# Kernel optimization log

Hardware: AMD Instinct MI355X
Metric: run time of the kernel (lower is better)

## Reference

```python
import jax, jax.numpy as jnp
import numpy as np

H = 768
NH = 12
HD = H // NH  # 64


def setup_inputs() -> dict:
    key = jax.random.key(0)
    ks = jax.random.split(key, 8)
    B, S = 4, 2048
    sc = 1.0 / np.sqrt(H)
    return {
        "hidden_states": jax.random.normal(ks[0], (B, S, H), dtype=jnp.float32),
        "attention_mask": jnp.zeros((B, 1, 1, S), dtype=jnp.float32),
        "Wq": jax.random.normal(ks[1], (H, H), dtype=jnp.float32) * sc,
        "bq": jnp.zeros((H,), dtype=jnp.float32),
        "Wk": jax.random.normal(ks[2], (H, H), dtype=jnp.float32) * sc,
        "bk": jnp.zeros((H,), dtype=jnp.float32),
        "Wv": jax.random.normal(ks[3], (H, H), dtype=jnp.float32) * sc,
        "bv": jnp.zeros((H,), dtype=jnp.float32),
    }


def _split_heads(x):
    # [B,S,H] -> [B,NH,S,HD]
    B, S, _ = x.shape
    return x.reshape(B, S, NH, HD).transpose(0, 2, 1, 3)


def reference(hidden_states, attention_mask, Wq, bq, Wk, bk, Wv, bv):
    q = _split_heads(hidden_states @ Wq + bq)
    k = _split_heads(hidden_states @ Wk + bk)
    v = _split_heads(hidden_states @ Wv + bv)
    # scores: [B,NH,S,S]
    scores = jnp.einsum("bhqd,bhkd->bhqk", q, k) / np.sqrt(HD)
    scores = scores + attention_mask
    probs = jax.nn.softmax(scores, axis=-1)  # dropout is identity in eval
    ctx = jnp.einsum("bhqk,bhkd->bhqd", probs, v)
    B, _, S, _ = ctx.shape
    return ctx.transpose(0, 2, 1, 3).reshape(B, S, H)
```

## Files before the change

kernel.cpp:

```cpp
#include <hip/hip_runtime.h>
#include <stdint.h>

typedef short bf16x8 __attribute__((ext_vector_type(8)));
typedef float f32x4  __attribute__((ext_vector_type(4)));
typedef float f32x16 __attribute__((ext_vector_type(16)));
typedef unsigned short u16;

#define B_  4
#define S_  2048
#define H_  768
#define NH_ 12
#define HD_ 64
#define NPROJ_N (3*H_)

static __device__ __forceinline__ u16 f2bf(float f) {
    union { float f; unsigned int u; } x; x.f = f;
    return (u16)((x.u + 0x8000u) >> 16);
}
static __device__ __forceinline__ bf16x8 ld8(const u16* p) {
    return *(const bf16x8*)(const void*)p;
}
static __device__ __forceinline__ void st8(u16* p, bf16x8 v) {
    *(bf16x8*)(void*)p = v;
}
static __device__ __forceinline__ void async_ld16(const u16* g, const short* l) {
    __builtin_amdgcn_global_load_lds(
        (__attribute__((address_space(1))) void*)g,
        (__attribute__((address_space(3))) void*)l,
        16, 0, 0);
}
static __device__ __forceinline__ unsigned cvtpk(float a, float b) {
    unsigned r;
    asm("v_cvt_pk_bf16_f32 %0, %1, %2" : "=v"(r) : "v"(a), "v"(b));
    return r;
}
static __device__ __forceinline__ void pl32swap(unsigned& a, unsigned& b) {
    asm("v_permlane32_swap_b32 %0, %1" : "+v"(a), "+v"(b));
}
static __device__ __forceinline__ bf16x8 mk8(unsigned a, unsigned b, unsigned c, unsigned d) {
    union { unsigned u[4]; bf16x8 v; } x;
    x.u[0] = a; x.u[1] = b; x.u[2] = c; x.u[3] = d;
    return x.v;
}

__global__ __launch_bounds__(256) void prep_kernel(const float* __restrict__ in,
                                                   u16* __restrict__ out,
                                                   const float* __restrict__ wq,
                                                   const float* __restrict__ wk,
                                                   const float* __restrict__ wv,
                                                   u16* __restrict__ wt,
                                                   const float* __restrict__ amask,
                                                   float* __restrict__ msc) {
    __shared__ float t[32][33];
    const int blk = blockIdx.x;
    const int tid = threadIdx.x;
    if (blk < 6144) {
        int i = (blk * 256 + tid) * 4;
        float4 v = *(const float4*)(in + i);
        ushort4 o;
        o.x = f2bf(v.x); o.y = f2bf(v.y); o.z = f2bf(v.z); o.w = f2bf(v.w);
        *(ushort4*)(out + i) = o;
    } else if (blk < 7872) {
        const int idx  = blk - 6144;
        const int proj = idx / 576;
        const int rem  = idx % 576;
        const int bx = rem % 24, by = rem / 24;
        const float* w = (proj == 0) ? wq : (proj == 1) ? wk : wv;
        u16* o = wt + (size_t)proj * H_ * H_;
        const int tx = tid & 31, ty = tid >> 5;
        const int n0 = bx * 32, k0 = by * 32;
        #pragma unroll
        for (int i = 0; i < 4; i++)
            t[ty + i * 8][tx] = w[(size_t)(k0 + ty + i * 8) * H_ + n0 + tx];
        __syncthreads();
        #pragma unroll
        for (int i = 0; i < 4; i++)
            o[(size_t)(n0 + ty + i * 8) * H_ + k0 + tx] = f2bf(t[tx][ty + i * 8]);
    } else {
        const int i = ((blk - 7872) * 256 + tid) * 8;
        float4 a0 = *(const float4*)(amask + i);
        float4 a1 = *(const float4*)(amask + i + 4);
        a0.x *= 1.44269504f; a0.y *= 1.44269504f; a0.z *= 1.44269504f; a0.w *= 1.44269504f;
        a1.x *= 1.44269504f; a1.y *= 1.44269504f; a1.z *= 1.44269504f; a1.w *= 1.44269504f;
        *(float4*)(msc + i)     = a0;
        *(float4*)(msc + i + 4) = a1;
    }
}

__global__ __launch_bounds__(256, 3) void qkv_gemm(const u16* __restrict__ A,
                                                   const u16* __restrict__ Wt,
                                                   const float* __restrict__ bq,
                                                   const float* __restrict__ bk,
                                                   const float* __restrict__ bv,
                                                   u16* __restrict__ qo,
                                                   u16* __restrict__ ko,
                                                   u16* __restrict__ vto) {
    __shared__ alignas(16) short SMEM[4][128 * 32];

    const int tid  = threadIdx.x;
    const int wave = tid >> 6;
    const int lane = tid & 63;
    const int quad = lane >> 4;
    const int l16  = lane & 15;
    const int wm   = wave & 1;
    const int wn   = wave >> 1;

    const int id  = blockIdx.x;
    const int xcd = id & 7;
    const int j   = id >> 3;
    const int mi  = j & 7;
    const int ni  = j >> 3;
    const int m0 = (xcd * 8 + mi) * 128;
    const int n0 = ni * 128;

    int stR[2], stC[2];
    #pragma unroll
    for (int jj = 0; jj < 2; jj++) {
        const int lc = jj * 256 + tid;
        stR[jj] = lc >> 2;
        stC[jj] = ((lc & 3) ^ ((lc >> 2) & 3)) * 8;
    }
    const int fx = (quad ^ (l16 & 3)) * 8;

    f32x4 acc[4][4];
    #pragma unroll
    for (int i = 0; i < 4; i++)
        #pragma unroll
        for (int jj = 0; jj < 4; jj++) acc[i][jj] = (f32x4)0.0f;

#define GSTAGE(kt_, buf_)                                                                     \
    do {                                                                                      \
        const int kk_ = (kt_) * 32;                                                           \
        _Pragma("unroll")                                                                     \
        for (int jj = 0; jj < 2; jj++) {                                                      \
            async_ld16(A  + (size_t)(m0 + stR[jj]) * H_ + kk_ + stC[jj],                      \
                       &SMEM[(buf_) * 2][(jj * 256 + tid) * 8]);                              \
            async_ld16(Wt + (size_t)(n0 + stR[jj]) * H_ + kk_ + stC[jj],                      \
                       &SMEM[(buf_) * 2 + 1][(jj * 256 + tid) * 8]);                          \
        }                                                                                     \
    } while (0)

    GSTAGE(0, 0);
    __syncthreads();

    for (int kt = 0; kt < 24; kt++) {
        const int cur = kt & 1;
        if (kt + 1 < 24) GSTAGE(kt + 1, cur ^ 1);
        const short* As = SMEM[cur * 2];
        const short* Bs = SMEM[cur * 2 + 1];
        bf16x8 af[4], bfr[4];
        #pragma unroll
        for (int i = 0; i < 4; i++)
            af[i] = *(const bf16x8*)(const void*)&As[(wm * 64 + i * 16 + l16) * 32 + fx];
        #pragma unroll
        for (int jj = 0; jj < 4; jj++)
            bfr[jj] = *(const bf16x8*)(const void*)&Bs[(wn * 64 + jj * 16 + l16) * 32 + fx];
        #pragma unroll
        for (int i = 0; i < 4; i++)
            #pragma unroll
            for (int jj = 0; jj < 4; jj++)
                acc[i][jj] = __builtin_amdgcn_mfma_f32_16x16x32_bf16(af[i], bfr[jj], acc[i][jj], 0, 0, 0);
        __syncthreads();
    }
#undef GSTAGE

    const int proj  = n0 / H_;
    const int hbase = (n0 % H_) >> 6;
    const float* bias = (proj == 0) ? bq : (proj == 1) ? bk : bv;
    u16* Ct = (u16*)SMEM;

    #pragma unroll
    for (int nj = 0; nj < 4; nj++) {
        const int nl = wn * 64 + nj * 16 + l16;
        const float bv_ = bias[(n0 % H_) + nl];
        #pragma unroll
        for (int mi2 = 0; mi2 < 4; mi2++) {
            #pragma unroll
            for (int r = 0; r < 4; r++) {
                const int ml = wm * 64 + mi2 * 16 + quad * 4 + r;
                const u16 val = f2bf(acc[mi2][nj][r] + bv_);
                if (proj < 2)
                    Ct[ml * 128 + ((nl + (ml & 15) * 8) & 127)] = val;
                else
                    Ct[nl * 128 + ((ml + (nl & 15) * 8) & 127)] = val;
            }
        }
    }
    __syncthreads();

    if (proj < 2) {
        u16* dst0 = (proj == 0) ? qo : ko;
        const int c = tid & 7;
        #pragma unroll
        for (int jj = 0; jj < 8; jj++) {
            const int idx = jj * 32 + (tid >> 3);
            const int ml = idx >> 1, h2 = idx & 1;
            const int nbase = h2 * 64 + c * 8;
            bf16x8 v8 = *(const bf16x8*)(const void*)&Ct[ml * 128 + ((nbase + (ml & 15) * 8) & 127)];
            const int m = m0 + ml;
            const int b = m >> 11, s = m & 2047;
            st8(dst0 + ((size_t)(b * NH_ + hbase + h2) * S_ + s) * HD_ + c * 8, v8);
        }
    } else {
        const int b = m0 >> 11;
        #pragma unroll
        for (int jj = 0; jj < 8; jj++) {
            const int nl = (tid >> 3) + (jj & 3) * 32;
            const int c  = (tid & 7) + (jj >> 2) * 8;
            bf16x8 v8 = *(const bf16x8*)(const void*)&Ct[nl * 128 + ((c * 8 + (nl & 15) * 8) & 127)];
            const int h2 = nl >> 6, d = nl & 63;
            st8(vto + ((size_t)(b * NH_ + hbase + h2) * HD_ + d) * S_ + (m0 & 2047) + c * 8, v8);
        }
    }
}

__global__ __launch_bounds__(256, 3) void attn_kernel(const u16* __restrict__ q,
                                                      const u16* __restrict__ k,
                                                      const u16* __restrict__ vt,
                                                      const float* __restrict__ msc,
                                                      float* __restrict__ out) {
    __shared__ alignas(16) short Ks[2][4096];
    __shared__ alignas(16) short Vs[2][4096];
    __shared__ alignas(16) float Ms[S_];

    const int tid  = threadIdx.x;
    const int wave = tid >> 6;
    const int lane = tid & 63;
    const int l32  = lane & 31;
    const int h    = lane >> 5;
    const int kh   = wave & 1;
    const int qg   = wave >> 1;

    const int bh = blockIdx.x;
    const int b  = bh / NH_;
    const int q0 = blockIdx.y * 128;
    const float C1 = 0.125f * 1.44269504f;

    {
        const float* mrow = msc + (size_t)b * S_;
        float4 a0 = *(const float4*)(mrow + tid * 8);
        float4 a1 = *(const float4*)(mrow + tid * 8 + 4);
        *(float4*)(Ms + tid * 8)     = a0;
        *(float4*)(Ms + tid * 8 + 4) = a1;
    }

    bf16x8 qf[2][4];
    #pragma unroll
    for (int qb = 0; qb < 2; qb++) {
        const u16* qrow = q + ((size_t)bh * S_ + q0 + qg * 64 + qb * 32 + l32) * HD_;
        #pragma unroll
        for (int i = 0; i < 4; i++) qf[qb][i] = ld8(qrow + i * 16 + h * 8);
    }

    const u16* kbase = k  + (size_t)bh * S_ * HD_;
    const u16* vbase = vt + (size_t)bh * HD_ * S_;

    const int sRow = tid >> 3;
    const int sCol = ((tid & 7) ^ (sRow & 7)) * 8;
    const int rx   = l32 & 7;

    float ls0 = 0.f, ls1 = 0.f;
    f32x16 oacc[2][2];
    #pragma unroll
    for (int qb = 0; qb < 2; qb++)
        #pragma unroll
        for (int dh = 0; dh < 2; dh++) oacc[qb][dh] = (f32x16)0.0f;

#define STAGE(kt_, buf_)                                                                           \
    do {                                                                                           \
        async_ld16(kbase + (size_t)(kt_) * 4096 + sRow * 64 + sCol,          &Ks[buf_][tid * 8]);  \
        async_ld16(kbase + (size_t)(kt_) * 4096 + (sRow + 32) * 64 + sCol,   &Ks[buf_][2048 + tid * 8]); \
        async_ld16(vbase + (size_t)sRow * S_ + (kt_) * 64 + sCol,            &Vs[buf_][tid * 8]);  \
        async_ld16(vbase + (size_t)(sRow + 32) * S_ + (kt_) * 64 + sCol,     &Vs[buf_][2048 + tid * 8]); \
    } while (0)

    STAGE(0, 0);
    __syncthreads();

    for (int kt = 0; kt < S_ / 64; kt++) {
        const int cur = kt & 1;
        if (kt + 1 < S_ / 64) STAGE(kt + 1, cur ^ 1);
        const short* Kc = Ks[cur];
        const short* Vc = Vs[cur];

        f32x16 s0 = (f32x16)0.0f;
        f32x16 s1 = (f32x16)0.0f;
        __builtin_amdgcn_s_setprio(1);
        #pragma unroll
        for (int i = 0; i < 4; i++) {
            bf16x8 kf = *(const bf16x8*)(const void*)&Kc[kh * 2048 + l32 * 64 + (((h + 2 * i) ^ rx) * 8)];
            s0 = __builtin_amdgcn_mfma_f32_32x32x16_bf16(kf, qf[0][i], s0, 0, 0, 0);
            s1 = __builtin_amdgcn_mfma_f32_32x32x16_bf16(kf, qf[1][i], s1, 0, 0, 0);
        }
        __builtin_amdgcn_s_setprio(0);

        unsigned w0[8], w1[8];
        #pragma unroll
        for (int c = 0; c < 4; c++) {
            const f32x4 mm = *(const f32x4*)&Ms[kt * 64 + kh * 32 + c * 8 + h * 4];
            const float p00 = __builtin_amdgcn_exp2f(__builtin_fmaf(s0[4*c+0], C1, mm[0]));
            const float p01 = __builtin_amdgcn_exp2f(__builtin_fmaf(s0[4*c+1], C1, mm[1]));
            const float p02 = __builtin_amdgcn_exp2f(__builtin_fmaf(s0[4*c+2], C1, mm[2]));
            const float p03 = __builtin_amdgcn_exp2f(__builtin_fmaf(s0[4*c+3], C1, mm[3]));
            const float p10 = __builtin_amdgcn_exp2f(__builtin_fmaf(s1[4*c+0], C1, mm[0]));
            const float p11 = __builtin_amdgcn_exp2f(__builtin_fmaf(s1[4*c+1], C1, mm[1]));
            const float p12 = __builtin_amdgcn_exp2f(__builtin_fmaf(s1[4*c+2], C1, mm[2]));
            const float p13 = __builtin_amdgcn_exp2f(__builtin_fmaf(s1[4*c+3], C1, mm[3]));
            w0[2*c]   = cvtpk(p00, p01);
            w0[2*c+1] = cvtpk(p02, p03);
            w1[2*c]   = cvtpk(p10, p11);
            w1[2*c+1] = cvtpk(p12, p13);
            ls0 += (p00 + p01) + (p02 + p03);
            ls1 += (p10 + p11) + (p12 + p13);
        }

        bf16x8 pa0[2], pa1[2];
        #pragma unroll
        for (int t = 0; t < 2; t++) {
            {
                unsigned a = w0[4*t+0], bb = w0[4*t+2];
                pl32swap(a, bb);
                unsigned c2 = w0[4*t+1], dd = w0[4*t+3];
                pl32swap(c2, dd);
                pa0[t] = mk8(a, c2, bb, dd);
            }
            {
                unsigned a = w1[4*t+0], bb = w1[4*t+2];
                pl32swap(a, bb);
                unsigned c2 = w1[4*t+1], dd = w1[4*t+3];
                pl32swap(c2, dd);
                pa1[t] = mk8(a, c2, bb, dd);
            }
        }

        __builtin_amdgcn_s_setprio(1);
        #pragma unroll
        for (int t = 0; t < 2; t++) {
            #pragma unroll
            for (int dh = 0; dh < 2; dh++) {
                bf16x8 vf = *(const bf16x8*)(const void*)&Vc[dh * 2048 + l32 * 64 + (((kh * 4 + 2 * t + h) ^ rx) * 8)];
                oacc[0][dh] = __builtin_amdgcn_mfma_f32_32x32x16_bf16(pa0[t], vf, oacc[0][dh], 0, 0, 0);
                oacc[1][dh] = __builtin_amdgcn_mfma_f32_32x32x16_bf16(pa1[t], vf, oacc[1][dh], 0, 0, 0);
            }
        }
        __builtin_amdgcn_s_setprio(0);
        __syncthreads();
    }
#undef STAGE

    ls0 += __shfl_xor(ls0, 32);
    ls1 += __shfl_xor(ls1, 32);

    float* R = qg ? (float*)Vs : (float*)Ks;

    if (kh == 1) {
        #pragma unroll
        for (int qb = 0; qb < 2; qb++)
            #pragma unroll
            for (int dh = 0; dh < 2; dh++)
                #pragma unroll
                for (int r = 0; r < 16; r++) {
                    const int qrow = (r & 3) + 8 * (r >> 2) + 4 * h;
                    R[(qb * 32 + qrow) * 64 + dh * 32 + l32] = oacc[qb][dh][r];
                }
        if (lane < 32) {
            Ms[qg * 64 + l32]      = ls0;
            Ms[qg * 64 + 32 + l32] = ls1;
        }
    }
    __syncthreads();

    if (kh == 0) {
        const float li0 = 1.0f / (ls0 + Ms[qg * 64 + l32]);
        const float li1 = 1.0f / (ls1 + Ms[qg * 64 + 32 + l32]);
        const int hh = bh % NH_;
        #pragma unroll
        for (int r = 0; r < 16; r++) {
            const int qrow = (r & 3) + 8 * (r >> 2) + 4 * h;
            const float lv0 = __shfl(li0, qrow);
            const float lv1 = __shfl(li1, qrow);
            #pragma unroll
            for (int dh = 0; dh < 2; dh++) {
                const int d = dh * 32 + l32;
                const int s0r = q0 + qg * 64 + qrow;
                out[((size_t)b * S_ + s0r) * H_ + hh * 64 + d] =
                    (oacc[0][dh][r] + R[qrow * 64 + d]) * lv0;
                out[((size_t)b * S_ + s0r + 32) * H_ + hh * 64 + d] =
                    (oacc[1][dh][r] + R[(32 + qrow) * 64 + d]) * lv1;
            }
        }
    }
}

extern "C" void kernel_launch(void* const* d_in, const int* in_sizes, int n_in,
                              void* d_out, int out_size, void* d_ws, size_t ws_size,
                              hipStream_t stream) {
    const float* hidden = (const float*)d_in[0];
    const float* amask  = (const float*)d_in[1];
    const float* Wq     = (const float*)d_in[2];
    const float* bq     = (const float*)d_in[3];
    const float* Wk     = (const float*)d_in[4];
    const float* bk     = (const float*)d_in[5];
    const float* Wv     = (const float*)d_in[6];
    const float* bv     = (const float*)d_in[7];
    float* out = (float*)d_out;

    char* ws = (char*)d_ws;
    const size_t sz_hidden = (size_t)B_ * S_ * H_ * 2;
    const size_t sz_wt     = (size_t)NPROJ_N * H_ * 2;
    const size_t sz_qkv    = (size_t)B_ * S_ * H_ * 2;

    u16* hid_bf = (u16*)(ws);
    u16* wt     = (u16*)(ws + sz_hidden);
    u16* qbuf   = (u16*)(ws + sz_hidden + sz_wt);
    u16* kbuf   = (u16*)(ws + sz_hidden + sz_wt + sz_qkv);
    u16* vtbuf  = (u16*)(ws + sz_hidden + sz_wt + 2 * sz_qkv);
    float* msc  = (float*)(ws + sz_hidden + sz_wt + 3 * sz_qkv);

    prep_kernel<<<dim3(6144 + 1728 + 4), dim3(256), 0, stream>>>(
        hidden, hid_bf, Wq, Wk, Wv, wt, amask, msc);
    qkv_gemm<<<dim3(1152), dim3(256), 0, stream>>>(
        hid_bf, wt, bq, bk, bv, qbuf, kbuf, vtbuf);
    attn_kernel<<<dim3(B_ * NH_, S_ / 128), dim3(256), 0, stream>>>(
        qbuf, kbuf, vtbuf, msc, out);
}
```

Before: 204.4 us.

## Split attention block into eight waves each owning 32 query rows

The attention kernel now launches 512 threads per block instead of 256. Each wave handles one 32-row query tile instead of two, so per-wave accumulators and registers are halved, and the K/V staging work is spread over twice as many threads. Launch bounds move to 512 threads with a higher occupancy target. This aims to raise latency hiding and occupancy, at the cost of less Q-fragment reuse per K/V LDS read and more LDS traffic per MFMA.

```diff
diff --git a/kernel.cpp b/kernel.cpp
--- a/kernel.cpp
+++ b/kernel.cpp
@@ -214,7 +214,7 @@
     }
 }
 
-__global__ __launch_bounds__(256, 3) void attn_kernel(const u16* __restrict__ q,
+__global__ __launch_bounds__(512, 4) void attn_kernel(const u16* __restrict__ q,
                                                       const u16* __restrict__ k,
                                                       const u16* __restrict__ vt,
                                                       const float* __restrict__ msc,
@@ -238,19 +238,14 @@
 
     {
         const float* mrow = msc + (size_t)b * S_;
-        float4 a0 = *(const float4*)(mrow + tid * 8);
-        float4 a1 = *(const float4*)(mrow + tid * 8 + 4);
-        *(float4*)(Ms + tid * 8)     = a0;
-        *(float4*)(Ms + tid * 8 + 4) = a1;
-    }
-
-    bf16x8 qf[2][4];
+        float4 a0 = *(const float4*)(mrow + tid * 4);
+        *(float4*)(Ms + tid * 4) = a0;
+    }
+
+    const u16* qrow = q + ((size_t)bh * S_ + q0 + qg * 32 + l32) * HD_;
+    bf16x8 qf[4];
     #pragma unroll
-    for (int qb = 0; qb < 2; qb++) {
-        const u16* qrow = q + ((size_t)bh * S_ + q0 + qg * 64 + qb * 32 + l32) * HD_;
-        #pragma unroll
-        for (int i = 0; i < 4; i++) qf[qb][i] = ld8(qrow + i * 16 + h * 8);
-    }
+    for (int i = 0; i < 4; i++) qf[i] = ld8(qrow + i * 16 + h * 8);
 
     const u16* kbase = k  + (size_t)bh * S_ * HD_;
     const u16* vbase = vt + (size_t)bh * HD_ * S_;
@@ -259,19 +254,15 @@
     const int sCol = ((tid & 7) ^ (sRow & 7)) * 8;
     const int rx   = l32 & 7;
 
-    float ls0 = 0.f, ls1 = 0.f;
-    f32x16 oacc[2][2];
-    #pragma unroll
-    for (int qb = 0; qb < 2; qb++)
-        #pragma unroll
-        for (int dh = 0; dh < 2; dh++) oacc[qb][dh] = (f32x16)0.0f;
-
-#define STAGE(kt_, buf_)                                                                           \
-    do {                                                                                           \
-        async_ld16(kbase + (size_t)(kt_) * 4096 + sRow * 64 + sCol,          &Ks[buf_][tid * 8]);  \
-        async_ld16(kbase + (size_t)(kt_) * 4096 + (sRow + 32) * 64 + sCol,   &Ks[buf_][2048 + tid * 8]); \
-        async_ld16(vbase + (size_t)sRow * S_ + (kt_) * 64 + sCol,            &Vs[buf_][tid * 8]);  \
-        async_ld16(vbase + (size_t)(sRow + 32) * S_ + (kt_) * 64 + sCol,     &Vs[buf_][2048 + tid * 8]); \
+    float ls = 0.f;
+    f32x16 oacc[2];
+    oacc[0] = (f32x16)0.0f;
+    oacc[1] = (f32x16)0.0f;
+
+#define STAGE(kt_, buf_)                                                                 \
+    do {                                                                                 \
+        async_ld16(kbase + (size_t)(kt_) * 4096 + sRow * 64 + sCol, &Ks[buf_][tid * 8]); \
+        async_ld16(vbase + (size_t)sRow * S_ + (kt_) * 64 + sCol,   &Vs[buf_][tid * 8]); \
     } while (0)
 
     STAGE(0, 0);
@@ -283,54 +274,36 @@
         const short* Kc = Ks[cur];
         const short* Vc = Vs[cur];
 
-        f32x16 s0 = (f32x16)0.0f;
-        f32x16 s1 = (f32x16)0.0f;
+        f32x16 s = (f32x16)0.0f;
         __builtin_amdgcn_s_setprio(1);
         #pragma unroll
         for (int i = 0; i < 4; i++) {
             bf16x8 kf = *(const bf16x8*)(const void*)&Kc[kh * 2048 + l32 * 64 + (((h + 2 * i) ^ rx) * 8)];
-            s0 = __builtin_amdgcn_mfma_f32_32x32x16_bf16(kf, qf[0][i], s0, 0, 0, 0);
-            s1 = __builtin_amdgcn_mfma_f32_32x32x16_bf16(kf, qf[1][i], s1, 0, 0, 0);
+            s = __builtin_amdgcn_mfma_f32_32x32x16_bf16(kf, qf[i], s, 0, 0, 0);
         }
         __builtin_amdgcn_s_setprio(0);
 
-        unsigned w0[8], w1[8];
+        unsigned w[8];
         #pragma unroll
         for (int c = 0; c < 4; c++) {
             const f32x4 mm = *(const f32x4*)&Ms[kt * 64 + kh * 32 + c * 8 + h * 4];
-            const float p00 = __builtin_amdgcn_exp2f(__builtin_fmaf(s0[4*c+0], C1, mm[0]));
-            const float p01 = __builtin_amdgcn_exp2f(__builtin_fmaf(s0[4*c+1], C1, mm[1]));
-            const float p02 = __builtin_amdgcn_exp2f(__builtin_fmaf(s0[4*c+2], C1, mm[2]));
-            const float p03 = __builtin_amdgcn_exp2f(__builtin_fmaf(s0[4*c+3], C1, mm[3]));
-            const float p10 = __builtin_amdgcn_exp2f(__builtin_fmaf(s1[4*c+0], C1, mm[0]));
-            const float p11 = __builtin_amdgcn_exp2f(__builtin_fmaf(s1[4*c+1], C1, mm[1]));
-            const float p12 = __builtin_amdgcn_exp2f(__builtin_fmaf(s1[4*c+2], C1, mm[2]));
-            const float p13 = __builtin_amdgcn_exp2f(__builtin_fmaf(s1[4*c+3], C1, mm[3]));
-            w0[2*c]   = cvtpk(p00, p01);
-            w0[2*c+1] = cvtpk(p02, p03);
-            w1[2*c]   = cvtpk(p10, p11);
-            w1[2*c+1] = cvtpk(p12, p13);
-            ls0 += (p00 + p01) + (p02 + p03);
-            ls1 += (p10 + p11) + (p12 + p13);
-        }
-
-        bf16x8 pa0[2], pa1[2];
+            const float p0 = __builtin_amdgcn_exp2f(__builtin_fmaf(s[4*c+0], C1, mm[0]));
+            const float p1 = __builtin_amdgcn_exp2f(__builtin_fmaf(s[4*c+1], C1, mm[1]));
+            const float p2 = __builtin_amdgcn_exp2f(__builtin_fmaf(s[4*c+2], C1, mm[2]));
+            const float p3 = __builtin_amdgcn_exp2f(__builtin_fmaf(s[4*c+3], C1, mm[3]));
+            w[2*c]   = cvtpk(p0, p1);
+            w[2*c+1] = cvtpk(p2, p3);
+            ls += (p0 + p1) + (p2 + p3);
+        }
+
+        bf16x8 pa[2];
         #pragma unroll
         for (int t = 0; t < 2; t++) {
-            {
-                unsigned a = w0[4*t+0], bb = w0[4*t+2];
-                pl32swap(a, bb);
-                unsigned c2 = w0[4*t+1], dd = w0[4*t+3];
-                pl32swap(c2, dd);
-                pa0[t] = mk8(a, c2, bb, dd);
-            }
-            {
-                unsigned a = w1[4*t+0], bb = w1[4*t+2];
-                pl32swap(a, bb);
-                unsigned c2 = w1[4*t+1], dd = w1[4*t+3];
-                pl32swap(c2, dd);
-                pa1[t] = mk8(a, c2, bb, dd);
-            }
+            unsigned a = w[4*t+0], bb = w[4*t+2];
+            pl32swap(a, bb);
+            unsigned c2 = w[4*t+1], dd = w[4*t+3];
+            pl32swap(c2, dd);
+            pa[t] = mk8(a, c2, bb, dd);
         }
 
         __builtin_amdgcn_s_setprio(1);
@@ -339,8 +312,7 @@
             #pragma unroll
             for (int dh = 0; dh < 2; dh++) {
                 bf16x8 vf = *(const bf16x8*)(const void*)&Vc[dh * 2048 + l32 * 64 + (((kh * 4 + 2 * t + h) ^ rx) * 8)];
-                oacc[0][dh] = __builtin_amdgcn_mfma_f32_32x32x16_bf16(pa0[t], vf, oacc[0][dh], 0, 0, 0);
-                oacc[1][dh] = __builtin_amdgcn_mfma_f32_32x32x16_bf16(pa1[t], vf, oacc[1][dh], 0, 0, 0);
+                oacc[dh] = __builtin_amdgcn_mfma_f32_32x32x16_bf16(pa[t], vf, oacc[dh], 0, 0, 0);
             }
         }
         __builtin_amdgcn_s_setprio(0);
@@ -348,45 +320,36 @@
     }
 #undef STAGE
 
-    ls0 += __shfl_xor(ls0, 32);
-    ls1 += __shfl_xor(ls1, 32);
-
-    float* R = qg ? (float*)Vs : (float*)Ks;
+    ls += __shfl_xor(ls, 32);
+
+    float* R = (qg == 0) ? (float*)&Ks[0][0] : (qg == 1) ? (float*)&Ks[1][0]
+             : (qg == 2) ? (float*)&Vs[0][0] : (float*)&Vs[1][0];
 
     if (kh == 1) {
         #pragma unroll
-        for (int qb = 0; qb < 2; qb++)
-            #pragma unroll
-            for (int dh = 0; dh < 2; dh++)
-                #pragma unroll
-                for (int r = 0; r < 16; r++) {
-                    const int qrow = (r & 3) + 8 * (r >> 2) + 4 * h;
-                    R[(qb * 32 + qrow) * 64 + dh * 32 + l32] = oacc[qb][dh][r];
-                }
-        if (lane < 32) {
-            Ms[qg * 64 + l32]      = ls0;
-            Ms[qg * 64 + 32 + l32] = ls1;
-        }
+        for (int dh = 0; dh < 2; dh++)
+            #pragma unroll
+            for (int r = 0; r < 16; r++) {
+                const int qr = (r & 3) + 8 * (r >> 2) + 4 * h;
+                R[qr * 64 + dh * 32 + l32] = oacc[dh][r];
+            }
+        if (lane < 32) Ms[qg * 32 + l32] = ls;
     }
     __syncthreads();
 
     if (kh == 0) {
-        const float li0 = 1.0f / (ls0 + Ms[qg * 64 + l32]);
-        const float li1 = 1.0f / (ls1 + Ms[qg * 64 + 32 + l32]);
+        const float li = 1.0f / (ls + Ms[qg * 32 + l32]);
         const int hh = bh % NH_;
         #pragma unroll
         for (int r = 0; r < 16; r++) {
-            const int qrow = (r & 3) + 8 * (r >> 2) + 4 * h;
-            const float lv0 = __shfl(li0, qrow);
-            const float lv1 = __shfl(li1, qrow);
+            const int qr = (r & 3) + 8 * (r >> 2) + 4 * h;
+            const float lv = __shfl(li, qr);
+            const int sidx = q0 + qg * 32 + qr;
             #pragma unroll
             for (int dh = 0; dh < 2; dh++) {
                 const int d = dh * 32 + l32;
-                const int s0r = q0 + qg * 64 + qrow;
-                out[((size_t)b * S_ + s0r) * H_ + hh * 64 + d] =
-                    (oacc[0][dh][r] + R[qrow * 64 + d]) * lv0;
-                out[((size_t)b * S_ + s0r + 32) * H_ + hh * 64 + d] =
-                    (oacc[1][dh][r] + R[(32 + qrow) * 64 + d]) * lv1;
+                out[((size_t)b * S_ + sidx) * H_ + hh * 64 + d] =
+                    (oacc[dh][r] + R[qr * 64 + d]) * lv;
             }
         }
     }
@@ -421,6 +384,6 @@
         hidden, hid_bf, Wq, Wk, Wv, wt, amask, msc);
     qkv_gemm<<<dim3(1152), dim3(256), 0, stream>>>(
         hid_bf, wt, bq, bk, bv, qbuf, kbuf, vtbuf);
-    attn_kernel<<<dim3(B_ * NH_, S_ / 128), dim3(256), 0, stream>>>(
+    attn_kernel<<<dim3(B_ * NH_, S_ / 128), dim3(512), 0, stream>>>(
         qbuf, kbuf, vtbuf, msc, out);
 }
```

New measurement: 209.2 us. 1.02x slower.

## Triple-buffer K tiles and use partial vmcnt waits in attention loop

Applied to the files above, without the earlier changes.

Splits staging of K and V tiles so K is prefetched two tiles ahead into a three-slot LDS ring while V stays double-buffered. Each iteration now waits with a partial vmcnt so the next tile's K load can stay in flight across the barrier, instead of a full __syncthreads drain. This adds 8 KB of LDS per block, which may reduce occupancy at launch_bounds(256,3), and correctness depends on the hand-counted vmcnt ordering.

```diff
diff --git a/kernel.cpp b/kernel.cpp
--- a/kernel.cpp
+++ b/kernel.cpp
@@ -219,7 +219,7 @@
                                                       const u16* __restrict__ vt,
                                                       const float* __restrict__ msc,
                                                       float* __restrict__ out) {
-    __shared__ alignas(16) short Ks[2][4096];
+    __shared__ alignas(16) short Ks[3][4096];
     __shared__ alignas(16) short Vs[2][4096];
     __shared__ alignas(16) float Ms[S_];
 
@@ -266,23 +266,18 @@
         #pragma unroll
         for (int dh = 0; dh < 2; dh++) oacc[qb][dh] = (f32x16)0.0f;
 
-#define STAGE(kt_, buf_)                                                                           \
+#define STAGE_K(kt_, bi_)                                                                          \
     do {                                                                                           \
-        async_ld16(kbase + (size_t)(kt_) * 4096 + sRow * 64 + sCol,          &Ks[buf_][tid * 8]);  \
-        async_ld16(kbase + (size_t)(kt_) * 4096 + (sRow + 32) * 64 + sCol,   &Ks[buf_][2048 + tid * 8]); \
-        async_ld16(vbase + (size_t)sRow * S_ + (kt_) * 64 + sCol,            &Vs[buf_][tid * 8]);  \
-        async_ld16(vbase + (size_t)(sRow + 32) * S_ + (kt_) * 64 + sCol,     &Vs[buf_][2048 + tid * 8]); \
+        async_ld16(kbase + (size_t)(kt_) * 4096 + sRow * 64 + sCol,        &Ks[bi_][tid * 8]);     \
+        async_ld16(kbase + (size_t)(kt_) * 4096 + (sRow + 32) * 64 + sCol, &Ks[bi_][2048 + tid * 8]); \
     } while (0)
-
-    STAGE(0, 0);
-    __syncthreads();
-
-    for (int kt = 0; kt < S_ / 64; kt++) {
-        const int cur = kt & 1;
-        if (kt + 1 < S_ / 64) STAGE(kt + 1, cur ^ 1);
-        const short* Kc = Ks[cur];
-        const short* Vc = Vs[cur];
-
+#define STAGE_V(kt_, bi_)                                                                          \
+    do {                                                                                           \
+        async_ld16(vbase + (size_t)sRow * S_ + (kt_) * 64 + sCol,          &Vs[bi_][tid * 8]);     \
+        async_ld16(vbase + (size_t)(sRow + 32) * S_ + (kt_) * 64 + sCol,   &Vs[bi_][2048 + tid * 8]); \
+    } while (0)
+
+    auto tile = [&](int kt, const short* Kc, const short* Vc) {
         f32x16 s0 = (f32x16)0.0f;
         f32x16 s1 = (f32x16)0.0f;
         __builtin_amdgcn_s_setprio(1);
@@ -344,9 +339,37 @@
             }
         }
         __builtin_amdgcn_s_setprio(0);
-        __syncthreads();
-    }
-#undef STAGE
+    };
+
+    STAGE_K(0, 0);
+    STAGE_K(1, 1);
+    STAGE_V(0, 0);
+    __syncthreads();
+
+    int cur = 0;
+    for (int kt = 0; kt < 31; kt++) {
+        STAGE_V(kt + 1, (kt + 1) & 1);
+        if (kt < 30) {
+            int kw = cur + 2; if (kw >= 3) kw -= 3;
+            STAGE_K(kt + 2, kw);
+        }
+
+        tile(kt, Ks[cur], Vs[kt & 1]);
+
+        if (kt < 30) {
+            asm volatile("s_waitcnt vmcnt(2)" ::: "memory");
+        } else {
+            asm volatile("s_waitcnt vmcnt(0)" ::: "memory");
+        }
+        __builtin_amdgcn_sched_barrier(0);
+        __builtin_amdgcn_s_barrier();
+        __builtin_amdgcn_sched_barrier(0);
+        cur = (cur + 1 == 3) ? 0 : cur + 1;
+    }
+    tile(31, Ks[cur], Vs[1]);
+    __syncthreads();
+#undef STAGE_K
+#undef STAGE_V
 
     ls0 += __shfl_xor(ls0, 32);
     ls1 += __shfl_xor(ls1, 32);
```

Measured after the change: 204.5 us. About the same (+0.1%).
